# Kernel tuning notes

Hardware: AMD Instinct MI355X
Metric: run time of the kernel (lower is better)

Reference implementation:

```python
import jax, jax.numpy as jnp
import numpy as np

B, N, T, D, E, H = 16, 512, 24, 64, 64, 64


def setup_inputs() -> dict:
    key = jax.random.key(0)
    ks = jax.random.split(key, 4)
    s = 1.0 / np.sqrt(D)
    return {
        "x": jax.random.normal(ks[0], (B, N, T, D), dtype=jnp.float32),
        "W1": jax.random.normal(ks[1], (D, E), dtype=jnp.float32) * s,
        "b1": jnp.zeros((E,), dtype=jnp.float32),
        "W2": jax.random.normal(ks[2], (D, E), dtype=jnp.float32) * s,
        "b2": jnp.zeros((E,), dtype=jnp.float32),
        "W": jax.random.normal(ks[3], (D, H), dtype=jnp.float32) * s,
        "b": jnp.zeros((H,), dtype=jnp.float32),
    }


def reference(x, W1, b1, W2, b2, W, b):
    # Original loops over t in python calling gcn_module(x[:, :, i, :]) and stacks;
    # here the identical per-timestep math is batched over the T axis.
    e1 = x @ W1 + b1                                   # [B,N,T,E]
    e2 = x @ W2 + b2                                   # [B,N,T,E]
    scores = jax.nn.relu(jnp.einsum("bite,bjte->btij", e1, e2))  # [B,T,N,N]
    A = jax.nn.softmax(scores, axis=-1)                # dynamic adjacency per (b,t)
    h = jnp.einsum("btij,bjtd->bitd", A, x)            # aggregate neighbors: [B,N,T,D]
    out = jax.nn.relu(h @ W + b)                       # [B,N,T,H]
    return out
```

## Files before the change

kernel.cpp:

```cpp
#include <hip/hip_runtime.h>


#define B_ 16
#define N_ 512
#define T_ 24
#define D_ 64
#define NT 8

typedef __attribute__((ext_vector_type(8))) short short8;
typedef __attribute__((ext_vector_type(4))) unsigned short u16x4;
typedef __attribute__((ext_vector_type(4))) float f32x4;

#define MFMA_BF16 __builtin_amdgcn_mfma_f32_16x16x32_bf16
#define WFIDX(q, cd, s, l) (((((q)*2 + (cd))*2 + (s))*64 + (l))*8)

#define OFF_E1 0u
#define OFF_E2 50331648u
#define OFF_XT 100663296u
#define OFF_WO 125829120u
#define WS_NEED 125845504u

__device__ __forceinline__ unsigned short f2bf(float f) {
    unsigned u = __float_as_uint(f);
    return (unsigned short)((u + 0x7FFFu + ((u >> 16) & 1u)) >> 16);
}
__device__ __forceinline__ float bf2f(unsigned short h) {
    return __uint_as_float(((unsigned)h) << 16);
}
__device__ __forceinline__ int XIDX(int j, int d) {
    return (d >> 4) * 1088 + (j >> 2) * 68 + ((j & 3) << 4) + (d & 15);
}
__device__ __forceinline__ int XTIDX(int d, int j) {
    return (j >> 4) * 1088 + (d >> 2) * 68 + ((d & 3) << 4) + (j & 15);
}
__device__ __forceinline__ int XIDX32(int i, int d) {
    return (d >> 4) * 544 + (i >> 2) * 68 + ((i & 3) << 4) + (d & 15);
}

__device__ __forceinline__ void stage_x(unsigned short* xb, unsigned short* xt,
                                        const float* src, int tid) {
    const int rs = T_ * D_;
    #pragma unroll
    for (int it = 0; it < 4; ++it) {
        int idx = tid + it * 256;
        int j = idx >> 4, d0 = (idx & 15) << 2;
        f32x4 v = *(const f32x4*)(src + (size_t)j * rs + d0);
        u16x4 hv, lv;
        #pragma unroll
        for (int k = 0; k < 4; ++k) {
            unsigned short h = f2bf(v[k]);
            hv[k] = h;
            lv[k] = f2bf(v[k] - bf2f(h));
        }
        int o = XIDX(j, d0);
        *(u16x4*)&xb[o] = hv;
        *(u16x4*)&xb[o + 4352] = lv;
        if (xt) {
            #pragma unroll
            for (int k = 0; k < 4; ++k)
                xt[XTIDX(d0 + k, j)] = hv[k];
        }
    }
}

__device__ __forceinline__ void gather_wfrag(unsigned short* wf, const float* Wg, int tid) {
    int lane = tid & 63, w = tid >> 6;
    #pragma unroll
    for (int k = 0; k < 2; ++k) {
        int pair = w * 2 + k;
        int q = pair >> 1, cd = pair & 1;
        int col = q * 16 + (lane & 15);
        short8 hf, lf;
        #pragma unroll
        for (int jj = 0; jj < 8; ++jj) {
            int row = cd * 32 + ((jj >> 2) << 4) + ((lane >> 4) << 2) + (jj & 3);
            float v = Wg[row * 64 + col];
            unsigned short h = f2bf(v);
            hf[jj] = (short)h;
            lf[jj] = (short)f2bf(v - bf2f(h));
        }
        *(short8*)&wf[WFIDX(q, cd, 0, lane)] = hf;
        *(short8*)&wf[WFIDX(q, cd, 1, lane)] = lf;
    }
}

__device__ __forceinline__ short8 xfrag(const unsigned short* xb, int row, int cd, int g) {
    u16x4 a = *(const u16x4*)&xb[XIDX(row, cd * 32 + (g << 2))];
    u16x4 b = *(const u16x4*)&xb[XIDX(row, cd * 32 + 16 + (g << 2))];
    short8 r;
    r[0] = (short)a[0]; r[1] = (short)a[1]; r[2] = (short)a[2]; r[3] = (short)a[3];
    r[4] = (short)b[0]; r[5] = (short)b[1]; r[6] = (short)b[2]; r[7] = (short)b[3];
    return r;
}
__device__ __forceinline__ short8 xfrag32(const unsigned short* p, int row, int cd, int g) {
    u16x4 a = *(const u16x4*)&p[XIDX32(row, cd * 32 + (g << 2))];
    u16x4 b = *(const u16x4*)&p[XIDX32(row, cd * 32 + 16 + (g << 2))];
    short8 r;
    r[0] = (short)a[0]; r[1] = (short)a[1]; r[2] = (short)a[2]; r[3] = (short)a[3];
    r[4] = (short)b[0]; r[5] = (short)b[1]; r[6] = (short)b[2]; r[7] = (short)b[3];
    return r;
}

__device__ __forceinline__ void repack_store(char* base, const f32x4* acc, int lane) {
    #pragma unroll
    for (int c = 0; c < 2; ++c) {
        short8 fh, fl;
        #pragma unroll
        for (int jj = 0; jj < 8; ++jj) {
            float v = acc[c * 2 + (jj >> 2)][jj & 3];
            unsigned short h = f2bf(v);
            fh[jj] = (short)h;
            fl[jj] = (short)f2bf(v - bf2f(h));
        }
        *(short8*)(base + (size_t)(c * 2 + 0) * 1024 + lane * 16) = fh;
        *(short8*)(base + (size_t)(c * 2 + 1) * 1024 + lane * 16) = fl;
    }
}

__global__ __launch_bounds__(256, 2)
void gcn_pre(const float* __restrict__ x,
             const float* __restrict__ W1, const float* __restrict__ b1,
             const float* __restrict__ W2, const float* __restrict__ b2,
             const float* __restrict__ Wo, char* __restrict__ ws)
{
    __shared__ __align__(16) char smem[59648];
    unsigned short* S1  = (unsigned short*)smem;
    unsigned short* XT  = (unsigned short*)(smem + 17408);
    unsigned short* WF1 = (unsigned short*)(smem + 26112);
    unsigned short* WF2 = (unsigned short*)(smem + 42496);
    float* b1s = (float*)(smem + 58880);
    float* b2s = (float*)(smem + 59136);

    const int tid = threadIdx.x;
    const int lane = tid & 63;
    const int w = tid >> 6;
    const int g = lane >> 4;
    const int li = lane & 15;

    const int bid = blockIdx.x;
    const int tile = bid & 7;
    const int bt = bid >> 3;
    const int b = bt / T_;
    const int t = bt - b * T_;
    const int r0 = tile * 64;

    const size_t rstride = (size_t)T_ * D_;
    const float* xbt = x + ((size_t)b * N_ * T_ + t) * D_;

    if (tid < 64) b1s[tid] = b1[tid];
    else if (tid < 128) b2s[tid - 64] = b2[tid - 64];

    gather_wfrag(WF1, W1, tid);
    gather_wfrag(WF2, W2, tid);
    stage_x(S1, XT, xbt + (size_t)r0 * rstride, tid);
    __syncthreads();

    f32x4 e1acc[4], e2acc[4];
    #pragma unroll
    for (int q = 0; q < 4; ++q) {
        e1acc[q] = (f32x4){0.f, 0.f, 0.f, 0.f};
        e2acc[q] = (f32x4){0.f, 0.f, 0.f, 0.f};
    }
    const int orow = w * 16 + li;
    #pragma unroll
    for (int cd = 0; cd < 2; ++cd) {
        short8 xh = xfrag(S1, orow, cd, g);
        short8 xl = xfrag(S1 + 4352, orow, cd, g);
        #pragma unroll
        for (int q = 0; q < 4; ++q) {
            short8 wh = *(const short8*)&WF1[WFIDX(q, cd, 0, lane)];
            short8 wl = *(const short8*)&WF1[WFIDX(q, cd, 1, lane)];
            e1acc[q] = MFMA_BF16(wh, xh, e1acc[q], 0, 0, 0);
            e1acc[q] = MFMA_BF16(wh, xl, e1acc[q], 0, 0, 0);
            e1acc[q] = MFMA_BF16(wl, xh, e1acc[q], 0, 0, 0);
            short8 vh = *(const short8*)&WF2[WFIDX(q, cd, 0, lane)];
            short8 vl = *(const short8*)&WF2[WFIDX(q, cd, 1, lane)];
            e2acc[q] = MFMA_BF16(vh, xh, e2acc[q], 0, 0, 0);
            e2acc[q] = MFMA_BF16(vh, xl, e2acc[q], 0, 0, 0);
            e2acc[q] = MFMA_BF16(vl, xh, e2acc[q], 0, 0, 0);
        }
    }
    #pragma unroll
    for (int q = 0; q < 4; ++q) {
        #pragma unroll
        for (int r = 0; r < 4; ++r) {
            e1acc[q][r] += b1s[q * 16 + g * 4 + r];
            e2acc[q][r] += b2s[q * 16 + g * 4 + r];
        }
    }
    const int grp = bt * 32 + tile * 4 + w;
    repack_store(ws + OFF_E1 + (size_t)grp * 4096, e1acc, lane);
    repack_store(ws + OFF_E2 + (size_t)grp * 4096, e2acc, lane);

    #pragma unroll
    for (int k = 0; k < 2; ++k) {
        int idx = w * 2 + k;
        int c = idx >> 2, n = idx & 3;
        short8 f = xfrag(XT, n * 16 + li, c, g);
        *(short8*)(ws + OFF_XT + (size_t)((bt * 8 + tile) * 8 + c * 4 + n) * 1024
                   + lane * 16) = f;
    }

    if (bid == 0) {
        #pragma unroll
        for (int k = 0; k < 2; ++k) {
            int pair = w * 2 + k;
            int q = pair >> 1, cd = pair & 1;
            int col = q * 16 + li;
            short8 hf, lf;
            #pragma unroll
            for (int jj = 0; jj < 8; ++jj) {
                int row = cd * 32 + ((jj >> 2) << 4) + (g << 2) + (jj & 3);
                float v = Wo[row * 64 + col];
                unsigned short h = f2bf(v);
                hf[jj] = (short)h;
                lf[jj] = (short)f2bf(v - bf2f(h));
            }
            *(short8*)(ws + OFF_WO + (size_t)((q * 2 + cd) * 2 + 0) * 1024 + lane * 16) = hf;
            *(short8*)(ws + OFF_WO + (size_t)((q * 2 + cd) * 2 + 1) * 1024 + lane * 16) = lf;
        }
    }
}

__global__ __launch_bounds__(64, 3)
void gcn_attn(const char* __restrict__ ws, const float* __restrict__ bo,
              float* __restrict__ out)
{
    __shared__ __align__(16) unsigned short hplane[4352];

    const int lane = threadIdx.x;
    const int g = lane >> 4;
    const int li = lane & 15;

    const int B0 = blockIdx.x;
    const int wid = (B0 & 7) * 768 + (B0 >> 3);
    const int bt = wid >> 4;
    const int iseg = wid & 15;
    const int b = bt / T_;
    const int t = bt - b * T_;

    const char* e1b = ws + OFF_E1 + (size_t)(bt * 32 + iseg * 2) * 4096;
    const char* e2b = ws + OFF_E2 + (size_t)bt * 131072;
    const char* xtb = ws + OFF_XT + (size_t)bt * 65536;

    short8 e1h[2][2], e1l[2][2];
    #pragma unroll
    for (int ig = 0; ig < 2; ++ig)
        #pragma unroll
        for (int c = 0; c < 2; ++c) {
            e1h[ig][c] = *(const short8*)(e1b + (size_t)(ig * 4 + c * 2 + 0) * 1024 + lane * 16);
            e1l[ig][c] = *(const short8*)(e1b + (size_t)(ig * 4 + c * 2 + 1) * 1024 + lane * 16);
        }

    f32x4 hacc[2][4];
    #pragma unroll
    for (int ig = 0; ig < 2; ++ig)
        #pragma unroll
        for (int n = 0; n < 4; ++n) hacc[ig][n] = (f32x4){0.f, 0.f, 0.f, 0.f};
    float m[2] = {0.f, 0.f}, l[2] = {0.f, 0.f};

    #pragma unroll 1
    for (int jc = 0; jc < 16; ++jc) {
        const char* eb = e2b + (size_t)jc * 8192;
        short8 ah[2][2], al[2][2];
        #pragma unroll
        for (int a = 0; a < 2; ++a)
            #pragma unroll
            for (int c = 0; c < 2; ++c) {
                ah[a][c] = *(const short8*)(eb + (size_t)(a * 4 + c * 2 + 0) * 1024 + lane * 16);
                al[a][c] = *(const short8*)(eb + (size_t)(a * 4 + c * 2 + 1) * 1024 + lane * 16);
            }
        short8 xt[4];
        const char* xb = xtb + (size_t)((jc >> 1) * 8 + (jc & 1) * 4) * 1024;
        #pragma unroll
        for (int n = 0; n < 4; ++n)
            xt[n] = *(const short8*)(xb + (size_t)n * 1024 + lane * 16);

        f32x4 st[2][2];
        #pragma unroll
        for (int a = 0; a < 2; ++a)
            #pragma unroll
            for (int ig = 0; ig < 2; ++ig) st[a][ig] = (f32x4){0.f, 0.f, 0.f, 0.f};
        #pragma unroll
        for (int a = 0; a < 2; ++a)
            #pragma unroll
            for (int ig = 0; ig < 2; ++ig)
                #pragma unroll
                for (int c = 0; c < 2; ++c) {
                    st[a][ig] = MFMA_BF16(ah[a][c], e1h[ig][c], st[a][ig], 0, 0, 0);
                    st[a][ig] = MFMA_BF16(al[a][c], e1h[ig][c], st[a][ig], 0, 0, 0);
                    st[a][ig] = MFMA_BF16(ah[a][c], e1l[ig][c], st[a][ig], 0, 0, 0);
                }

        #pragma unroll
        for (int ig = 0; ig < 2; ++ig) {
            float tm = 0.f;
            #pragma unroll
            for (int a = 0; a < 2; ++a)
                #pragma unroll
                for (int r = 0; r < 4; ++r) {
                    float s = fmaxf(st[a][ig][r], 0.f);
                    st[a][ig][r] = s;
                    tm = fmaxf(tm, s);
                }
            tm = fmaxf(tm, __shfl_xor(tm, 16));
            tm = fmaxf(tm, __shfl_xor(tm, 32));
            if (!__all(tm - m[ig] <= 8.f)) {
                float mn = fmaxf(m[ig], tm);
                float corr = __expf(m[ig] - mn);
                m[ig] = mn;
                l[ig] *= corr;
                #pragma unroll
                for (int r = 0; r < 4; ++r) {
                    float sc = __shfl(corr, g * 4 + r);
                    #pragma unroll
                    for (int n = 0; n < 4; ++n) hacc[ig][n][r] *= sc;
                }
            }
            float ps = 0.f;
            #pragma unroll
            for (int a = 0; a < 2; ++a)
                #pragma unroll
                for (int r = 0; r < 4; ++r) {
                    float p = __expf(st[a][ig][r] - m[ig]);
                    st[a][ig][r] = p;
                    ps += p;
                }
            ps += __shfl_xor(ps, 16);
            ps += __shfl_xor(ps, 32);
            l[ig] += ps;
        }

        #pragma unroll
        for (int ig = 0; ig < 2; ++ig) {
            short8 pa;
            #pragma unroll
            for (int jj = 0; jj < 8; ++jj)
                pa[jj] = (short)f2bf(st[jj >> 2][ig][jj & 3]);
            #pragma unroll
            for (int n = 0; n < 4; ++n)
                hacc[ig][n] = MFMA_BF16(pa, xt[n], hacc[ig][n], 0, 0, 0);
        }
    }

    #pragma unroll
    for (int ig = 0; ig < 2; ++ig) {
        float linv = 1.0f / l[ig];
        #pragma unroll
        for (int r = 0; r < 4; ++r) {
            float lr = __shfl(linv, g * 4 + r);
            #pragma unroll
            for (int n = 0; n < 4; ++n) {
                float v = hacc[ig][n][r] * lr;
                unsigned short h = f2bf(v);
                int o = XIDX32(ig * 16 + g * 4 + r, n * 16 + li);
                hplane[o] = h;
                hplane[o + 2176] = f2bf(v - bf2f(h));
            }
        }
    }
    __syncthreads();

    f32x4 oacc[2][4];
    #pragma unroll
    for (int ig = 0; ig < 2; ++ig)
        #pragma unroll
        for (int q = 0; q < 4; ++q) oacc[ig][q] = (f32x4){0.f, 0.f, 0.f, 0.f};
    #pragma unroll
    for (int ig = 0; ig < 2; ++ig)
        #pragma unroll
        for (int cd = 0; cd < 2; ++cd) {
            short8 ahh = xfrag32(hplane, ig * 16 + li, cd, g);
            short8 alo = xfrag32(hplane + 2176, ig * 16 + li, cd, g);
            #pragma unroll
            for (int q = 0; q < 4; ++q) {
                short8 wh = *(const short8*)(ws + OFF_WO
                              + (size_t)((q * 2 + cd) * 2 + 0) * 1024 + lane * 16);
                short8 wl = *(const short8*)(ws + OFF_WO
                              + (size_t)((q * 2 + cd) * 2 + 1) * 1024 + lane * 16);
                oacc[ig][q] = MFMA_BF16(ahh, wh, oacc[ig][q], 0, 0, 0);
                oacc[ig][q] = MFMA_BF16(alo, wh, oacc[ig][q], 0, 0, 0);
                oacc[ig][q] = MFMA_BF16(ahh, wl, oacc[ig][q], 0, 0, 0);
            }
        }

    float boq[4];
    #pragma unroll
    for (int q = 0; q < 4; ++q) boq[q] = bo[q * 16 + li];

    const size_t rstride = (size_t)T_ * D_;
    float* obt = out + ((size_t)b * N_ * T_ + t) * D_;
    const int i0 = iseg * 32;
    #pragma unroll
    for (int ig = 0; ig < 2; ++ig)
        #pragma unroll
        for (int q = 0; q < 4; ++q)
            #pragma unroll
            for (int r = 0; r < 4; ++r) {
                float v = fmaxf(oacc[ig][q][r] + boq[q], 0.f);
                obt[(size_t)(i0 + ig * 16 + g * 4 + r) * rstride + q * 16 + li] = v;
            }
}

__global__ __launch_bounds__(256, 2)
void gcn_mfma(const float* __restrict__ x,
              const float* __restrict__ W1, const float* __restrict__ b1,
              const float* __restrict__ W2, const float* __restrict__ b2,
              const float* __restrict__ Wo, const float* __restrict__ bo,
              float* __restrict__ out)
{
    __shared__ __align__(16) char smem[60672];
    unsigned short* S1 = (unsigned short*)smem;
    unsigned short* S2 = (unsigned short*)(smem + 17408);
    unsigned short* XT = (unsigned short*)(smem + 34816);
    unsigned short* SH = (unsigned short*)(smem + 43520);
    float* b1s = (float*)(smem + 59904);
    float* b2s = (float*)(smem + 60160);
    float* bos = (float*)(smem + 60416);

    const int tid = threadIdx.x;
    const int lane = tid & 63;
    const int w = tid >> 6;
    const int g = lane >> 4;
    const int li = lane & 15;

    const int bid = blockIdx.x;
    const int tile = bid & (NT - 1);
    const int bt = bid >> 3;
    const int b = bt / T_;
    const int t = bt - b * T_;
    const int r0 = tile * 64;

    const size_t rstride = (size_t)T_ * D_;
    const float* xbt = x + ((size_t)b * N_ * T_ + t) * D_;

    if (tid < 64) b1s[tid] = b1[tid];
    else if (tid < 128) b2s[tid - 64] = b2[tid - 64];
    else if (tid < 192) bos[tid - 128] = bo[tid - 128];

    gather_wfrag(S2, W1, tid);
    stage_x(S1, nullptr, xbt + (size_t)r0 * rstride, tid);
    __syncthreads();

    f32x4 eacc[4];
    #pragma unroll
    for (int q = 0; q < 4; ++q) eacc[q] = (f32x4){0.f, 0.f, 0.f, 0.f};
    const int orow = w * 16 + li;
    #pragma unroll
    for (int cd = 0; cd < 2; ++cd) {
        short8 xh = xfrag(S1, orow, cd, g);
        short8 xl = xfrag(S1 + 4352, orow, cd, g);
        #pragma unroll
        for (int q = 0; q < 4; ++q) {
            short8 wh = *(const short8*)&S2[WFIDX(q, cd, 0, lane)];
            short8 wl = *(const short8*)&S2[WFIDX(q, cd, 1, lane)];
            eacc[q] = MFMA_BF16(wh, xh, eacc[q], 0, 0, 0);
            eacc[q] = MFMA_BF16(wh, xl, eacc[q], 0, 0, 0);
            eacc[q] = MFMA_BF16(wl, xh, eacc[q], 0, 0, 0);
        }
    }
    short8 e1h[2], e1l[2];
    #pragma unroll
    for (int q = 0; q < 4; ++q) {
        #pragma unroll
        for (int r = 0; r < 4; ++r) eacc[q][r] += b1s[q * 16 + g * 4 + r];
    }
    #pragma unroll
    for (int c = 0; c < 2; ++c) {
        #pragma unroll
        for (int jj = 0; jj < 8; ++jj) {
            float v = eacc[c * 2 + (jj >> 2)][jj & 3];
            unsigned short h = f2bf(v);
            e1h[c][jj] = (short)h;
            e1l[c][jj] = (short)f2bf(v - bf2f(h));
        }
    }
    __syncthreads();
    gather_wfrag(S1, W2, tid);

    f32x4 hacc[4];
    #pragma unroll
    for (int n = 0; n < 4; ++n) hacc[n] = (f32x4){0.f, 0.f, 0.f, 0.f};
    float mrun = 0.f, lsum = 0.f;

    #pragma unroll 1
    for (int jt8 = 0; jt8 < NT; ++jt8) {
        __syncthreads();
        stage_x(S2, XT, xbt + (size_t)(jt8 * 64) * rstride, tid);
        __syncthreads();

        f32x4 e2[4];
        #pragma unroll
        for (int q = 0; q < 4; ++q) e2[q] = (f32x4){0.f, 0.f, 0.f, 0.f};
        #pragma unroll
        for (int cd = 0; cd < 2; ++cd) {
            short8 xh = xfrag(S2, orow, cd, g);
            short8 xl = xfrag(S2 + 4352, orow, cd, g);
            #pragma unroll
            for (int q = 0; q < 4; ++q) {
                short8 wh = *(const short8*)&S1[WFIDX(q, cd, 0, lane)];
                short8 wl = *(const short8*)&S1[WFIDX(q, cd, 1, lane)];
                e2[q] = MFMA_BF16(wh, xh, e2[q], 0, 0, 0);
                e2[q] = MFMA_BF16(wh, xl, e2[q], 0, 0, 0);
                e2[q] = MFMA_BF16(wl, xh, e2[q], 0, 0, 0);
            }
        }
        #pragma unroll
        for (int q = 0; q < 4; ++q) {
            #pragma unroll
            for (int r = 0; r < 4; ++r) e2[q][r] += b2s[q * 16 + g * 4 + r];
        }
        #pragma unroll
        for (int c = 0; c < 2; ++c) {
            short8 fh, fl;
            #pragma unroll
            for (int jj = 0; jj < 8; ++jj) {
                float v = e2[c * 2 + (jj >> 2)][jj & 3];
                unsigned short h = f2bf(v);
                fh[jj] = (short)h;
                fl[jj] = (short)f2bf(v - bf2f(h));
            }
            *(short8*)&SH[WFIDX(w, c, 0, lane)] = fh;
            *(short8*)&SH[WFIDX(w, c, 1, lane)] = fl;
        }
        __syncthreads();

        f32x4 st[4];
        #pragma unroll
        for (int jt = 0; jt < 4; ++jt) st[jt] = (f32x4){0.f, 0.f, 0.f, 0.f};
        #pragma unroll
        for (int jt = 0; jt < 4; ++jt) {
            #pragma unroll
            for (int c = 0; c < 2; ++c) {
                short8 ah = *(const short8*)&SH[WFIDX(jt, c, 0, lane)];
                short8 al = *(const short8*)&SH[WFIDX(jt, c, 1, lane)];
                st[jt] = MFMA_BF16(ah, e1h[c], st[jt], 0, 0, 0);
                st[jt] = MFMA_BF16(ah, e1l[c], st[jt], 0, 0, 0);
                st[jt] = MFMA_BF16(al, e1h[c], st[jt], 0, 0, 0);
            }
        }
        float tm = 0.f;
        #pragma unroll
        for (int jt = 0; jt < 4; ++jt) {
            #pragma unroll
            for (int r = 0; r < 4; ++r) {
                float s = fmaxf(st[jt][r], 0.f);
                st[jt][r] = s;
                tm = fmaxf(tm, s);
            }
        }
        tm = fmaxf(tm, __shfl_xor(tm, 16));
        tm = fmaxf(tm, __shfl_xor(tm, 32));
        float mn = fmaxf(mrun, tm);
        float corr = __expf(mrun - mn);
        float ps = 0.f;
        #pragma unroll
        for (int jt = 0; jt < 4; ++jt) {
            #pragma unroll
            for (int r = 0; r < 4; ++r) {
                float p = __expf(st[jt][r] - mn);
                st[jt][r] = p;
                ps += p;
            }
        }
        ps += __shfl_xor(ps, 16);
        ps += __shfl_xor(ps, 32);
        lsum = lsum * corr + ps;
        mrun = mn;
        float sc0 = __shfl(corr, g * 4 + 0);
        float sc1 = __shfl(corr, g * 4 + 1);
        float sc2 = __shfl(corr, g * 4 + 2);
        float sc3 = __shfl(corr, g * 4 + 3);
        #pragma unroll
        for (int n = 0; n < 4; ++n) {
            hacc[n][0] *= sc0; hacc[n][1] *= sc1; hacc[n][2] *= sc2; hacc[n][3] *= sc3;
        }

        #pragma unroll
        for (int c = 0; c < 2; ++c) {
            short8 pa;
            #pragma unroll
            for (int jj = 0; jj < 8; ++jj)
                pa[jj] = (short)f2bf(st[c * 2 + (jj >> 2)][jj & 3]);
            #pragma unroll
            for (int n = 0; n < 4; ++n) {
                short8 xb = xfrag(XT, n * 16 + li, c, g);
                hacc[n] = MFMA_BF16(pa, xb, hacc[n], 0, 0, 0);
            }
        }
    }

    float linv = 1.0f / lsum;
    float l0 = __shfl(linv, g * 4 + 0);
    float l1 = __shfl(linv, g * 4 + 1);
    float l2 = __shfl(linv, g * 4 + 2);
    float l3 = __shfl(linv, g * 4 + 3);
    __syncthreads();
    #pragma unroll
    for (int n = 0; n < 4; ++n) {
        float lr[4] = {l0, l1, l2, l3};
        #pragma unroll
        for (int r = 0; r < 4; ++r) {
            float v = hacc[n][r] * lr[r];
            unsigned short h = f2bf(v);
            int o = XIDX(w * 16 + g * 4 + r, n * 16 + li);
            S1[o] = h;
            S1[o + 4352] = f2bf(v - bf2f(h));
        }
    }
    gather_wfrag(S2, Wo, tid);
    __syncthreads();

    f32x4 oacc[4];
    #pragma unroll
    for (int n = 0; n < 4; ++n) oacc[n] = (f32x4){0.f, 0.f, 0.f, 0.f};
    #pragma unroll
    for (int cd = 0; cd < 2; ++cd) {
        short8 ah = xfrag(S1, orow, cd, g);
        short8 al = xfrag(S1 + 4352, orow, cd, g);
        #pragma unroll
        for (int n = 0; n < 4; ++n) {
            short8 wh = *(const short8*)&S2[WFIDX(n, cd, 0, lane)];
            short8 wl = *(const short8*)&S2[WFIDX(n, cd, 1, lane)];
            oacc[n] = MFMA_BF16(ah, wh, oacc[n], 0, 0, 0);
            oacc[n] = MFMA_BF16(al, wh, oacc[n], 0, 0, 0);
            oacc[n] = MFMA_BF16(ah, wl, oacc[n], 0, 0, 0);
        }
    }
    float* obt = out + ((size_t)b * N_ * T_ + t) * D_;
    #pragma unroll
    for (int n = 0; n < 4; ++n) {
        #pragma unroll
        for (int r = 0; r < 4; ++r) {
            float v = fmaxf(oacc[n][r] + bos[n * 16 + li], 0.f);
            obt[(size_t)(r0 + w * 16 + g * 4 + r) * rstride + n * 16 + li] = v;
        }
    }
}

extern "C" void kernel_launch(void* const* d_in, const int* in_sizes, int n_in,
                              void* d_out, int out_size, void* d_ws, size_t ws_size,
                              hipStream_t stream) {
    const float* x  = (const float*)d_in[0];
    const float* W1 = (const float*)d_in[1];
    const float* b1 = (const float*)d_in[2];
    const float* W2 = (const float*)d_in[3];
    const float* b2 = (const float*)d_in[4];
    const float* Wo = (const float*)d_in[5];
    const float* bo = (const float*)d_in[6];
    float* out = (float*)d_out;

    if (ws_size >= (size_t)WS_NEED) {
        char* ws = (char*)d_ws;
        gcn_pre<<<dim3(B_ * T_ * NT), dim3(256), 0, stream>>>(x, W1, b1, W2, b2, Wo, ws);
        gcn_attn<<<dim3(B_ * T_ * 16), dim3(64), 0, stream>>>(ws, bo, out);
    } else {
        gcn_mfma<<<dim3(B_ * T_ * NT), dim3(256), 0, stream>>>(x, W1, b1, W2, b2, Wo, bo, out);
    }
}
```

Baseline: 219.3 us.

## Hoist weight fragment prep, use exp2 softmax, pair waves per attention block

```diff
diff --git a/kernel.cpp b/kernel.cpp
--- a/kernel.cpp
+++ b/kernel.cpp
@@ -6,6 +6,7 @@
 #define T_ 24
 #define D_ 64
 #define NT 8
+#define LOG2E 1.44269504088896f
 
 typedef __attribute__((ext_vector_type(8))) short short8;
 typedef __attribute__((ext_vector_type(4))) unsigned short u16x4;
@@ -17,8 +18,10 @@
 #define OFF_E1 0u
 #define OFF_E2 50331648u
 #define OFF_XT 100663296u
-#define OFF_WO 125829120u
-#define WS_NEED 125845504u
+#define OFF_W1F 125829120u
+#define OFF_W2F 125845504u
+#define OFF_WOF 125861888u
+#define WS_NEED 125878272u
 
 __device__ __forceinline__ unsigned short f2bf(float f) {
     unsigned u = __float_as_uint(f);
@@ -117,19 +120,43 @@
     }
 }
 
+__global__ __launch_bounds__(256, 1)
+void gcn_wf(const float* __restrict__ W1, const float* __restrict__ W2,
+            const float* __restrict__ Wo, char* __restrict__ ws)
+{
+    const int lane = threadIdx.x & 63;
+    const int w = threadIdx.x >> 6;
+    const float* Wg = (blockIdx.x == 0) ? W1 : (blockIdx.x == 1) ? W2 : Wo;
+    char* dst = ws + ((blockIdx.x == 0) ? OFF_W1F : (blockIdx.x == 1) ? OFF_W2F : OFF_WOF);
+    #pragma unroll
+    for (int k = 0; k < 2; ++k) {
+        int pair = w * 2 + k;
+        int q = pair >> 1, cd = pair & 1;
+        int col = q * 16 + (lane & 15);
+        short8 hf, lf;
+        #pragma unroll
+        for (int jj = 0; jj < 8; ++jj) {
+            int row = cd * 32 + ((jj >> 2) << 4) + ((lane >> 4) << 2) + (jj & 3);
+            float v = Wg[row * 64 + col];
+            unsigned short h = f2bf(v);
+            hf[jj] = (short)h;
+            lf[jj] = (short)f2bf(v - bf2f(h));
+        }
+        *(short8*)(dst + (size_t)(pair * 2 + 0) * 1024 + lane * 16) = hf;
+        *(short8*)(dst + (size_t)(pair * 2 + 1) * 1024 + lane * 16) = lf;
+    }
+}
+
 __global__ __launch_bounds__(256, 2)
 void gcn_pre(const float* __restrict__ x,
-             const float* __restrict__ W1, const float* __restrict__ b1,
-             const float* __restrict__ W2, const float* __restrict__ b2,
-             const float* __restrict__ Wo, char* __restrict__ ws)
+             const float* __restrict__ b1, const float* __restrict__ b2,
+             char* __restrict__ ws)
 {
-    __shared__ __align__(16) char smem[59648];
-    unsigned short* S1  = (unsigned short*)smem;
-    unsigned short* XT  = (unsigned short*)(smem + 17408);
-    unsigned short* WF1 = (unsigned short*)(smem + 26112);
-    unsigned short* WF2 = (unsigned short*)(smem + 42496);
-    float* b1s = (float*)(smem + 58880);
-    float* b2s = (float*)(smem + 59136);
+    __shared__ __align__(16) char smem[26624];
+    unsigned short* S1 = (unsigned short*)smem;
+    unsigned short* XT = (unsigned short*)(smem + 17408);
+    float* b1s = (float*)(smem + 26112);
+    float* b2s = (float*)(smem + 26368);
 
     const int tid = threadIdx.x;
     const int lane = tid & 63;
@@ -150,10 +177,11 @@
     if (tid < 64) b1s[tid] = b1[tid];
     else if (tid < 128) b2s[tid - 64] = b2[tid - 64];
 
-    gather_wfrag(WF1, W1, tid);
-    gather_wfrag(WF2, W2, tid);
     stage_x(S1, XT, xbt + (size_t)r0 * rstride, tid);
     __syncthreads();
+
+    const char* w1f = ws + OFF_W1F;
+    const char* w2f = ws + OFF_W2F;
 
     f32x4 e1acc[4], e2acc[4];
     #pragma unroll
@@ -168,13 +196,14 @@
         short8 xl = xfrag(S1 + 4352, orow, cd, g);
         #pragma unroll
         for (int q = 0; q < 4; ++q) {
-            short8 wh = *(const short8*)&WF1[WFIDX(q, cd, 0, lane)];
-            short8 wl = *(const short8*)&WF1[WFIDX(q, cd, 1, lane)];
+            size_t fo = (size_t)((q * 2 + cd) * 2) * 1024 + lane * 16;
+            short8 wh = *(const short8*)(w1f + fo);
+            short8 wl = *(const short8*)(w1f + fo + 1024);
             e1acc[q] = MFMA_BF16(wh, xh, e1acc[q], 0, 0, 0);
             e1acc[q] = MFMA_BF16(wh, xl, e1acc[q], 0, 0, 0);
             e1acc[q] = MFMA_BF16(wl, xh, e1acc[q], 0, 0, 0);
-            short8 vh = *(const short8*)&WF2[WFIDX(q, cd, 0, lane)];
-            short8 vl = *(const short8*)&WF2[WFIDX(q, cd, 1, lane)];
+            short8 vh = *(const short8*)(w2f + fo);
+            short8 vl = *(const short8*)(w2f + fo + 1024);
             e2acc[q] = MFMA_BF16(vh, xh, e2acc[q], 0, 0, 0);
             e2acc[q] = MFMA_BF16(vh, xl, e2acc[q], 0, 0, 0);
             e2acc[q] = MFMA_BF16(vl, xh, e2acc[q], 0, 0, 0);
@@ -184,7 +213,7 @@
     for (int q = 0; q < 4; ++q) {
         #pragma unroll
         for (int r = 0; r < 4; ++r) {
-            e1acc[q][r] += b1s[q * 16 + g * 4 + r];
+            e1acc[q][r] = (e1acc[q][r] + b1s[q * 16 + g * 4 + r]) * LOG2E;
             e2acc[q][r] += b2s[q * 16 + g * 4 + r];
         }
     }
@@ -200,42 +229,24 @@
         *(short8*)(ws + OFF_XT + (size_t)((bt * 8 + tile) * 8 + c * 4 + n) * 1024
                    + lane * 16) = f;
     }
-
-    if (bid == 0) {
-        #pragma unroll
-        for (int k = 0; k < 2; ++k) {
-            int pair = w * 2 + k;
-            int q = pair >> 1, cd = pair & 1;
-            int col = q * 16 + li;
-            short8 hf, lf;
-            #pragma unroll
-            for (int jj = 0; jj < 8; ++jj) {
-                int row = cd * 32 + ((jj >> 2) << 4) + (g << 2) + (jj & 3);
-                float v = Wo[row * 64 + col];
-                unsigned short h = f2bf(v);
-                hf[jj] = (short)h;
-                lf[jj] = (short)f2bf(v - bf2f(h));
-            }
-            *(short8*)(ws + OFF_WO + (size_t)((q * 2 + cd) * 2 + 0) * 1024 + lane * 16) = hf;
-            *(short8*)(ws + OFF_WO + (size_t)((q * 2 + cd) * 2 + 1) * 1024 + lane * 16) = lf;
-        }
-    }
-}
-
-__global__ __launch_bounds__(64, 3)
+}
+
+__global__ __launch_bounds__(128, 3)
 void gcn_attn(const char* __restrict__ ws, const float* __restrict__ bo,
               float* __restrict__ out)
 {
-    __shared__ __align__(16) unsigned short hplane[4352];
-
-    const int lane = threadIdx.x;
+    __shared__ __align__(16) unsigned short hplane[8704];
+
+    const int tid = threadIdx.x;
+    const int lane = tid & 63;
+    const int w = tid >> 6;
     const int g = lane >> 4;
     const int li = lane & 15;
 
     const int B0 = blockIdx.x;
-    const int wid = (B0 & 7) * 768 + (B0 >> 3);
-    const int bt = wid >> 4;
-    const int iseg = wid & 15;
+    const int wid = (B0 & 7) * 384 + (B0 >> 3);
+    const int bt = wid >> 3;
+    const int iseg = (wid & 7) * 2 + w;
     const int b = bt / T_;
     const int t = bt - b * T_;
 
@@ -257,11 +268,12 @@
     for (int ig = 0; ig < 2; ++ig)
         #pragma unroll
         for (int n = 0; n < 4; ++n) hacc[ig][n] = (f32x4){0.f, 0.f, 0.f, 0.f};
-    float m[2] = {0.f, 0.f}, l[2] = {0.f, 0.f};
+    float m0 = 0.f, m1 = 0.f, l0 = 0.f, l1 = 0.f;
 
     #pragma unroll 1
     for (int jc = 0; jc < 16; ++jc) {
         const char* eb = e2b + (size_t)jc * 8192;
+        const char* xb = xtb + (size_t)jc * 4096;
         short8 ah[2][2], al[2][2];
         #pragma unroll
         for (int a = 0; a < 2; ++a)
@@ -271,7 +283,6 @@
                 al[a][c] = *(const short8*)(eb + (size_t)(a * 4 + c * 2 + 1) * 1024 + lane * 16);
             }
         short8 xt[4];
-        const char* xb = xtb + (size_t)((jc >> 1) * 8 + (jc & 1) * 4) * 1024;
         #pragma unroll
         for (int n = 0; n < 4; ++n)
             xt[n] = *(const short8*)(xb + (size_t)n * 1024 + lane * 16);
@@ -281,6 +292,7 @@
         for (int a = 0; a < 2; ++a)
             #pragma unroll
             for (int ig = 0; ig < 2; ++ig) st[a][ig] = (f32x4){0.f, 0.f, 0.f, 0.f};
+        __builtin_amdgcn_s_setprio(1);
         #pragma unroll
         for (int a = 0; a < 2; ++a)
             #pragma unroll
@@ -291,72 +303,81 @@
                     st[a][ig] = MFMA_BF16(al[a][c], e1h[ig][c], st[a][ig], 0, 0, 0);
                     st[a][ig] = MFMA_BF16(ah[a][c], e1l[ig][c], st[a][ig], 0, 0, 0);
                 }
-
-        #pragma unroll
-        for (int ig = 0; ig < 2; ++ig) {
-            float tm = 0.f;
-            #pragma unroll
-            for (int a = 0; a < 2; ++a)
+        __builtin_amdgcn_s_setprio(0);
+
+        float tm0 = 0.f, tm1 = 0.f;
+        #pragma unroll
+        for (int a = 0; a < 2; ++a)
+            #pragma unroll
+            for (int r = 0; r < 4; ++r) {
+                float s0 = fmaxf(st[a][0][r], 0.f);
+                float s1 = fmaxf(st[a][1][r], 0.f);
+                st[a][0][r] = s0; st[a][1][r] = s1;
+                tm0 = fmaxf(tm0, s0); tm1 = fmaxf(tm1, s1);
+            }
+        float u0 = __shfl_xor(tm0, 16), u1 = __shfl_xor(tm1, 16);
+        tm0 = fmaxf(tm0, u0); tm1 = fmaxf(tm1, u1);
+        u0 = __shfl_xor(tm0, 32); u1 = __shfl_xor(tm1, 32);
+        tm0 = fmaxf(tm0, u0); tm1 = fmaxf(tm1, u1);
+        bool ok = (tm0 - m0 <= 11.54f) && (tm1 - m1 <= 11.54f);
+        if (!__all(ok)) {
+            float mn0 = fmaxf(m0, tm0), mn1 = fmaxf(m1, tm1);
+            float c0 = exp2f(m0 - mn0), c1 = exp2f(m1 - mn1);
+            m0 = mn0; m1 = mn1; l0 *= c0; l1 *= c1;
+            #pragma unroll
+            for (int r = 0; r < 4; ++r) {
+                float sc0 = __shfl(c0, g * 4 + r);
+                float sc1 = __shfl(c1, g * 4 + r);
                 #pragma unroll
-                for (int r = 0; r < 4; ++r) {
-                    float s = fmaxf(st[a][ig][r], 0.f);
-                    st[a][ig][r] = s;
-                    tm = fmaxf(tm, s);
+                for (int n = 0; n < 4; ++n) {
+                    hacc[0][n][r] *= sc0;
+                    hacc[1][n][r] *= sc1;
                 }
-            tm = fmaxf(tm, __shfl_xor(tm, 16));
-            tm = fmaxf(tm, __shfl_xor(tm, 32));
-            if (!__all(tm - m[ig] <= 8.f)) {
-                float mn = fmaxf(m[ig], tm);
-                float corr = __expf(m[ig] - mn);
-                m[ig] = mn;
-                l[ig] *= corr;
-                #pragma unroll
-                for (int r = 0; r < 4; ++r) {
-                    float sc = __shfl(corr, g * 4 + r);
-                    #pragma unroll
-                    for (int n = 0; n < 4; ++n) hacc[ig][n][r] *= sc;
-                }
-            }
-            float ps = 0.f;
-            #pragma unroll
-            for (int a = 0; a < 2; ++a)
-                #pragma unroll
-                for (int r = 0; r < 4; ++r) {
-                    float p = __expf(st[a][ig][r] - m[ig]);
-                    st[a][ig][r] = p;
-                    ps += p;
-                }
-            ps += __shfl_xor(ps, 16);
-            ps += __shfl_xor(ps, 32);
-            l[ig] += ps;
-        }
-
+            }
+        }
+        float ps0 = 0.f, ps1 = 0.f;
+        #pragma unroll
+        for (int a = 0; a < 2; ++a)
+            #pragma unroll
+            for (int r = 0; r < 4; ++r) {
+                float p0 = exp2f(st[a][0][r] - m0);
+                float p1 = exp2f(st[a][1][r] - m1);
+                st[a][0][r] = p0; st[a][1][r] = p1;
+                ps0 += p0; ps1 += p1;
+            }
+        ps0 += __shfl_xor(ps0, 16); ps1 += __shfl_xor(ps1, 16);
+        ps0 += __shfl_xor(ps0, 32); ps1 += __shfl_xor(ps1, 32);
+        l0 += ps0; l1 += ps1;
+
+        __builtin_amdgcn_s_setprio(1);
         #pragma unroll
         for (int ig = 0; ig < 2; ++ig) {
             short8 pa;
             #pragma unroll
             for (int jj = 0; jj < 8; ++jj)
-                pa[jj] = (short)f2bf(st[jj >> 2][ig][jj & 3]);
+                pa[jj] = (short)(__float_as_uint(st[jj >> 2][ig][jj & 3]) >> 16);
             #pragma unroll
             for (int n = 0; n < 4; ++n)
                 hacc[ig][n] = MFMA_BF16(pa, xt[n], hacc[ig][n], 0, 0, 0);
         }
-    }
-
-    #pragma unroll
-    for (int ig = 0; ig < 2; ++ig) {
-        float linv = 1.0f / l[ig];
-        #pragma unroll
-        for (int r = 0; r < 4; ++r) {
-            float lr = __shfl(linv, g * 4 + r);
-            #pragma unroll
-            for (int n = 0; n < 4; ++n) {
-                float v = hacc[ig][n][r] * lr;
-                unsigned short h = f2bf(v);
-                int o = XIDX32(ig * 16 + g * 4 + r, n * 16 + li);
-                hplane[o] = h;
-                hplane[o + 2176] = f2bf(v - bf2f(h));
-            }
+        __builtin_amdgcn_s_setprio(0);
+    }
+
+    unsigned short* hp = hplane + w * 4352;
+    float li0 = 1.0f / l0, li1 = 1.0f / l1;
+    #pragma unroll
+    for (int r = 0; r < 4; ++r) {
+        float lr0 = __shfl(li0, g * 4 + r);
+        float lr1 = __shfl(li1, g * 4 + r);
+        #pragma unroll
+        for (int n = 0; n < 4; ++n) {
+            float v0 = hacc[0][n][r] * lr0;
+            float v1 = hacc[1][n][r] * lr1;
+            unsigned short h0 = f2bf(v0), h1 = f2bf(v1);
+            int o0 = XIDX32(g * 4 + r, n * 16 + li);
+            int o1 = XIDX32(16 + g * 4 + r, n * 16 + li);
+            hp[o0] = h0; hp[o0 + 2176] = f2bf(v0 - bf2f(h0));
+            hp[o1] = h1; hp[o1 + 2176] = f2bf(v1 - bf2f(h1));
         }
     }
     __syncthreads();
@@ -370,13 +391,13 @@
     for (int ig = 0; ig < 2; ++ig)
         #pragma unroll
         for (int cd = 0; cd < 2; ++cd) {
-            short8 ahh = xfrag32(hplane, ig * 16 + li, cd, g);
-            short8 alo = xfrag32(hplane + 2176, ig * 16 + li, cd, g);
+            short8 ahh = xfrag32(hp, ig * 16 + li, cd, g);
+            short8 alo = xfrag32(hp + 2176, ig * 16 + li, cd, g);
             #pragma unroll
             for (int q = 0; q < 4; ++q) {
-                short8 wh = *(const short8*)(ws + OFF_WO
+                short8 wh = *(const short8*)(ws + OFF_WOF
                               + (size_t)((q * 2 + cd) * 2 + 0) * 1024 + lane * 16);
-                short8 wl = *(const short8*)(ws + OFF_WO
+                short8 wl = *(const short8*)(ws + OFF_WOF
                               + (size_t)((q * 2 + cd) * 2 + 1) * 1024 + lane * 16);
                 oacc[ig][q] = MFMA_BF16(ahh, wh, oacc[ig][q], 0, 0, 0);
                 oacc[ig][q] = MFMA_BF16(alo, wh, oacc[ig][q], 0, 0, 0);
@@ -652,8 +673,9 @@
 
     if (ws_size >= (size_t)WS_NEED) {
         char* ws = (char*)d_ws;
-        gcn_pre<<<dim3(B_ * T_ * NT), dim3(256), 0, stream>>>(x, W1, b1, W2, b2, Wo, ws);
-        gcn_attn<<<dim3(B_ * T_ * 16), dim3(64), 0, stream>>>(ws, bo, out);
+        gcn_wf<<<dim3(3), dim3(256), 0, stream>>>(W1, W2, Wo, ws);
+        gcn_pre<<<dim3(B_ * T_ * NT), dim3(256), 0, stream>>>(x, b1, b2, ws);
+        gcn_attn<<<dim3(B_ * T_ * NT), dim3(128), 0, stream>>>(ws, bo, out);
     } else {
         gcn_mfma<<<dim3(B_ * T_ * NT), dim3(256), 0, stream>>>(x, W1, b1, W2, b2, Wo, bo, out);
     }
```

Result: no change. 215.7 us (-1.7%).
